# Optimization experiments

Hardware: AMD Instinct MI355X
Metric: run time of the kernel (lower is better)

Reference implementation:

```python
import jax, jax.numpy as jnp
import numpy as np


def _pairwise_sq_dist(a, b):
    # a: (B,N,D), b: (B,M,D) -> (B,N,M) squared euclidean distances
    # matmul trick matching torch.cdist (clamped at 0 before implicit sqrt)
    a2 = jnp.sum(a * a, axis=-1)  # (B,N)
    b2 = jnp.sum(b * b, axis=-1)  # (B,M)
    ab = jnp.einsum('bnd,bmd->bnm', a, b)  # (B,N,M)
    d2 = a2[:, :, None] + b2[:, None, :] - 2.0 * ab
    return jnp.maximum(d2, 0.0)


def setup_inputs() -> dict:
    key = jax.random.key(0)
    k1, k2 = jax.random.split(key)
    B, N, M, D = 8, 8192, 8192, 3
    gts = jax.random.normal(k1, (B, N, D), dtype=jnp.float32)
    preds = jax.random.normal(k2, (B, M, D), dtype=jnp.float32)
    return {"gts": gts, "preds": preds}


def reference(gts, preds):
    d2 = _pairwise_sq_dist(gts, preds)           # (B,N,M)
    min_g2p = jnp.min(d2, axis=2)                # (B,N) nearest pred for each gt
    min_p2g = jnp.min(d2, axis=1)                # (B,M) nearest gt for each pred
    return jnp.mean(min_g2p) + jnp.mean(min_p2g)
```

## Files before the change

kernel.cpp:

```cpp
#include <hip/hip_runtime.h>
#include <math.h>


#define BB 8
#define NPTS 8192
#define ROWS 512
#define CH 1024
#define NPAIR (CH / 64)

typedef __attribute__((ext_vector_type(8)))  short short8;
typedef __attribute__((ext_vector_type(16))) float float16;

#define ONE_BF16 ((short)0x3F80)

__device__ inline unsigned short bf16rn(float f) {
    unsigned int u = __float_as_uint(f);
    u += 0x7FFFu + ((u >> 16) & 1u);
    return (unsigned short)(u >> 16);
}
__device__ inline float bf2f(unsigned short h) {
    return __uint_as_float(((unsigned int)h) << 16);
}
__device__ inline float min3f(float a, float b, float c) {
    return fminf(fminf(a, b), c);
}
__device__ inline float min16(const float16 d) {
    float t0 = min3f(d[0],  d[1],  d[2]);
    float t1 = min3f(d[3],  d[4],  d[5]);
    float t2 = min3f(d[6],  d[7],  d[8]);
    float t3 = min3f(d[9],  d[10], d[11]);
    float t4 = min3f(d[12], d[13], d[14]);
    return fminf(min3f(t0, t1, t2), min3f(t3, t4, d[15]));
}

#define DPP_FMIN(v, CTRL) do {                                                \
    int _s = __builtin_amdgcn_update_dpp(__float_as_int(v), __float_as_int(v),\
                                         (CTRL), 0xf, 0xf, false);            \
    (v) = fminf((v), __int_as_float(_s)); } while (0)

__device__ inline void packB(float x, float y, float z, short8& lo, short8& hi) {
    float w = x * x + y * y + z * z;
    unsigned short xh = bf16rn(x), yh = bf16rn(y), zh = bf16rn(z);
    unsigned short xl = bf16rn(x - bf2f(xh));
    unsigned short yl = bf16rn(y - bf2f(yh));
    unsigned short zl = bf16rn(z - bf2f(zh));
    unsigned short wh = bf16rn(w), wl = bf16rn(w - bf2f(wh));
    lo[0]=(short)xh; lo[1]=(short)yh; lo[2]=(short)zh; lo[3]=(short)xl;
    lo[4]=(short)yl; lo[5]=(short)zl; lo[6]=(short)xh; lo[7]=(short)yh;
    hi[0]=(short)zh; hi[1]=ONE_BF16;  hi[2]=ONE_BF16;  hi[3]=(short)wh;
    hi[4]=(short)wl; hi[5]=0;         hi[6]=0;         hi[7]=0;
}
__device__ inline void packA(float x, float y, float z, short8& lo, short8& hi) {
    float w = x * x + y * y + z * z;
    float mx = -2.0f * x, my = -2.0f * y, mz = -2.0f * z;
    unsigned short xh = bf16rn(mx), yh = bf16rn(my), zh = bf16rn(mz);
    unsigned short xl = bf16rn(mx - bf2f(xh));
    unsigned short yl = bf16rn(my - bf2f(yh));
    unsigned short zl = bf16rn(mz - bf2f(zh));
    unsigned short wh = bf16rn(w), wl = bf16rn(w - bf2f(wh));
    lo[0]=(short)xh; lo[1]=(short)yh; lo[2]=(short)zh; lo[3]=(short)xh;
    lo[4]=(short)yh; lo[5]=(short)zh; lo[6]=(short)xl; lo[7]=(short)yl;
    hi[0]=(short)zl; hi[1]=(short)wh; hi[2]=(short)wl; hi[3]=ONE_BF16;
    hi[4]=ONE_BF16;  hi[5]=0;         hi[6]=0;         hi[7]=0;
}

__global__ __launch_bounds__(512, 4) void chamfer_main(
    const float* __restrict__ gts, const float* __restrict__ preds,
    unsigned int* __restrict__ minn, unsigned int* __restrict__ minp)
{
    __shared__ short8 sB[2][CH];

    const int b       = blockIdx.z;
    const int rowBase = blockIdx.x * ROWS;
    const int colBase = blockIdx.y * CH;
    const int tid  = threadIdx.x;
    const int lane = tid & 63;
    const int wave = tid >> 6;
    const int h    = lane >> 5;
    const int c    = lane & 31;

    for (int i = tid; i < CH; i += 512) {
        const float* p = preds + ((size_t)b * NPTS + colBase + i) * 3;
        short8 lo, hi;
        packB(p[0], p[1], p[2], lo, hi);
        sB[0][i] = lo; sB[1][i] = hi;
    }

    short8 a[2];
    {
        const float* g = gts + ((size_t)b * NPTS + rowBase + wave * 64 + c) * 3;
#pragma unroll
        for (int r = 0; r < 2; ++r) {
            short8 lo, hi;
            packA(g[r*96], g[r*96+1], g[r*96+2], lo, hi);
            a[r] = h ? hi : lo;
        }
    }

    float16 zacc;
#pragma unroll
    for (int q = 0; q < 16; ++q) zacc[q] = 0.0f;

    const float kInf = __builtin_inff();
    float rm[2][16];
#pragma unroll
    for (int r = 0; r < 2; ++r)
#pragma unroll
        for (int q = 0; q < 16; ++q) rm[r][q] = kInf;

    __syncthreads();

    unsigned int* minp_b = minp + (size_t)b * NPTS + colBase;
    const short8* myB = &sB[h][c];

#pragma unroll 2
    for (int tp = 0; tp < NPAIR; ++tp) {
        short8 b0 = myB[tp * 64];
        short8 b1 = myB[tp * 64 + 32];
        float16 d0 = __builtin_amdgcn_mfma_f32_32x32x16_bf16(a[0], b0, zacc, 0, 0, 0);
        float16 d1 = __builtin_amdgcn_mfma_f32_32x32x16_bf16(a[0], b1, zacc, 0, 0, 0);
#pragma unroll
        for (int q = 0; q < 16; ++q) rm[0][q] = min3f(rm[0][q], d0[q], d1[q]);
        float c0 = min16(d0);
        float c1 = min16(d1);
        d0 = __builtin_amdgcn_mfma_f32_32x32x16_bf16(a[1], b0, zacc, 0, 0, 0);
        d1 = __builtin_amdgcn_mfma_f32_32x32x16_bf16(a[1], b1, zacc, 0, 0, 0);
#pragma unroll
        for (int q = 0; q < 16; ++q) rm[1][q] = min3f(rm[1][q], d0[q], d1[q]);
        c0 = fminf(c0, min16(d0));
        c1 = fminf(c1, min16(d1));
        c0 = fminf(c0, __shfl_xor(c0, 32));
        c1 = fminf(c1, __shfl_xor(c1, 32));
        float cv = h ? c1 : c0;
        atomicMin(&minp_b[tp * 64 + lane], __float_as_uint(fmaxf(cv, 0.0f)));
    }

#pragma unroll
    for (int r = 0; r < 2; ++r)
#pragma unroll
        for (int q = 0; q < 16; ++q) {
            float v = rm[r][q];
            DPP_FMIN(v, 0x111);
            DPP_FMIN(v, 0x112);
            DPP_FMIN(v, 0x114);
            DPP_FMIN(v, 0x118);
            DPP_FMIN(v, 0x142);
            rm[r][q] = v;
        }
    if ((lane & 31) == 31) {
        unsigned int* mb = minn + (size_t)b * NPTS + rowBase + wave * 64;
#pragma unroll
        for (int r = 0; r < 2; ++r)
#pragma unroll
            for (int q = 0; q < 16; ++q) {
                int row = r * 32 + (q & 3) + 8 * (q >> 2) + 4 * h;
                atomicMin(&mb[row], __float_as_uint(fmaxf(rm[r][q], 0.0f)));
            }
    }
}

__global__ void chamfer_reduce(const unsigned int* __restrict__ minn,
                               const unsigned int* __restrict__ minp,
                               float* __restrict__ accum,
                               unsigned int* __restrict__ ticket,
                               float* __restrict__ out)
{
    const int idx = blockIdx.x * blockDim.x + threadIdx.x;
    const int stride = gridDim.x * blockDim.x;

    float s0 = 0.0f, s1 = 0.0f;
    for (int i = idx; i < BB * NPTS; i += stride) s0 += __uint_as_float(minn[i]);
    for (int i = idx; i < BB * NPTS; i += stride) s1 += __uint_as_float(minp[i]);

#pragma unroll
    for (int m = 1; m < 64; m <<= 1) {
        s0 += __shfl_xor(s0, m, 64);
        s1 += __shfl_xor(s1, m, 64);
    }
    __shared__ float w0[4], w1[4];
    if ((threadIdx.x & 63) == 0) {
        w0[threadIdx.x >> 6] = s0;
        w1[threadIdx.x >> 6] = s1;
    }
    __syncthreads();
    if (threadIdx.x == 0) {
        atomicAdd(&accum[0], w0[0] + w0[1] + w0[2] + w0[3]);
        atomicAdd(&accum[1], w1[0] + w1[1] + w1[2] + w1[3]);
        __threadfence();
        unsigned int old = atomicAdd(ticket, 1u);
        unsigned int G = gridDim.x;
        if (old == 0xAAAAAAAAu + G - 1u || old == G - 1u) {
            float a0 = atomicAdd(&accum[0], 0.0f);
            float a1 = atomicAdd(&accum[1], 0.0f);
            out[0] = a0 / (float)(BB * NPTS) + a1 / (float)(BB * NPTS);
        }
    }
}

extern "C" void kernel_launch(void* const* d_in, const int* in_sizes, int n_in,
                              void* d_out, int out_size, void* d_ws, size_t ws_size,
                              hipStream_t stream) {
    const float* gts   = (const float*)d_in[0];
    const float* preds = (const float*)d_in[1];
    float* out = (float*)d_out;

    unsigned int* minn   = (unsigned int*)d_ws;
    unsigned int* minp   = minn + (size_t)BB * NPTS;
    float*        accum  = (float*)(minp + (size_t)BB * NPTS);
    unsigned int* ticket = (unsigned int*)(accum + 2);

    dim3 grid(NPTS / ROWS, NPTS / CH, BB);
    chamfer_main<<<grid, 512, 0, stream>>>(gts, preds, minn, minp);

    chamfer_reduce<<<64, 256, 0, stream>>>(minn, minp, accum, ticket, out);
}
```

Measured before the change: 105.1 us.

## Compute each chamfer direction in separate blocks instead of column-min atomics

Doubles the grid so that one half of the blocks computes gt-to-pred row minima and the other half computes pred-to-gt row minima, with the roles of the two point sets swapped. This drops the per-iteration column reductions, cross-half shuffles and global atomicMin from the inner loop. In exchange, every distance tile is computed twice, doubling MFMA work. The loop unroll factor is also raised from 2 to 4.

```diff
diff --git a/kernel.cpp b/kernel.cpp
--- a/kernel.cpp
+++ b/kernel.cpp
@@ -23,14 +23,6 @@
 }
 __device__ inline float min3f(float a, float b, float c) {
     return fminf(fminf(a, b), c);
-}
-__device__ inline float min16(const float16 d) {
-    float t0 = min3f(d[0],  d[1],  d[2]);
-    float t1 = min3f(d[3],  d[4],  d[5]);
-    float t2 = min3f(d[6],  d[7],  d[8]);
-    float t3 = min3f(d[9],  d[10], d[11]);
-    float t4 = min3f(d[12], d[13], d[14]);
-    return fminf(min3f(t0, t1, t2), min3f(t3, t4, d[15]));
 }
 
 #define DPP_FMIN(v, CTRL) do {                                                \
@@ -70,7 +62,9 @@
 {
     __shared__ short8 sB[2][CH];
 
-    const int b       = blockIdx.z;
+    const int zz      = blockIdx.z;
+    const int b       = zz >> 1;
+    const int dir     = zz & 1;
     const int rowBase = blockIdx.x * ROWS;
     const int colBase = blockIdx.y * CH;
     const int tid  = threadIdx.x;
@@ -79,8 +73,12 @@
     const int h    = lane >> 5;
     const int c    = lane & 31;
 
+    const float* Arr = dir ? preds : gts;
+    const float* Brr = dir ? gts : preds;
+    unsigned int* outMin = (dir ? minp : minn) + (size_t)b * NPTS;
+
     for (int i = tid; i < CH; i += 512) {
-        const float* p = preds + ((size_t)b * NPTS + colBase + i) * 3;
+        const float* p = Brr + ((size_t)b * NPTS + colBase + i) * 3;
         short8 lo, hi;
         packB(p[0], p[1], p[2], lo, hi);
         sB[0][i] = lo; sB[1][i] = hi;
@@ -88,7 +86,7 @@
 
     short8 a[2];
     {
-        const float* g = gts + ((size_t)b * NPTS + rowBase + wave * 64 + c) * 3;
+        const float* g = Arr + ((size_t)b * NPTS + rowBase + wave * 64 + c) * 3;
 #pragma unroll
         for (int r = 0; r < 2; ++r) {
             short8 lo, hi;
@@ -110,10 +108,9 @@
 
     __syncthreads();
 
-    unsigned int* minp_b = minp + (size_t)b * NPTS + colBase;
     const short8* myB = &sB[h][c];
 
-#pragma unroll 2
+#pragma unroll 4
     for (int tp = 0; tp < NPAIR; ++tp) {
         short8 b0 = myB[tp * 64];
         short8 b1 = myB[tp * 64 + 32];
@@ -121,18 +118,10 @@
         float16 d1 = __builtin_amdgcn_mfma_f32_32x32x16_bf16(a[0], b1, zacc, 0, 0, 0);
 #pragma unroll
         for (int q = 0; q < 16; ++q) rm[0][q] = min3f(rm[0][q], d0[q], d1[q]);
-        float c0 = min16(d0);
-        float c1 = min16(d1);
-        d0 = __builtin_amdgcn_mfma_f32_32x32x16_bf16(a[1], b0, zacc, 0, 0, 0);
-        d1 = __builtin_amdgcn_mfma_f32_32x32x16_bf16(a[1], b1, zacc, 0, 0, 0);
-#pragma unroll
-        for (int q = 0; q < 16; ++q) rm[1][q] = min3f(rm[1][q], d0[q], d1[q]);
-        c0 = fminf(c0, min16(d0));
-        c1 = fminf(c1, min16(d1));
-        c0 = fminf(c0, __shfl_xor(c0, 32));
-        c1 = fminf(c1, __shfl_xor(c1, 32));
-        float cv = h ? c1 : c0;
-        atomicMin(&minp_b[tp * 64 + lane], __float_as_uint(fmaxf(cv, 0.0f)));
+        float16 d2 = __builtin_amdgcn_mfma_f32_32x32x16_bf16(a[1], b0, zacc, 0, 0, 0);
+        float16 d3 = __builtin_amdgcn_mfma_f32_32x32x16_bf16(a[1], b1, zacc, 0, 0, 0);
+#pragma unroll
+        for (int q = 0; q < 16; ++q) rm[1][q] = min3f(rm[1][q], d2[q], d3[q]);
     }
 
 #pragma unroll
@@ -148,7 +137,7 @@
             rm[r][q] = v;
         }
     if ((lane & 31) == 31) {
-        unsigned int* mb = minn + (size_t)b * NPTS + rowBase + wave * 64;
+        unsigned int* mb = outMin + rowBase + wave * 64;
 #pragma unroll
         for (int r = 0; r < 2; ++r)
 #pragma unroll
@@ -209,7 +198,7 @@
     float*        accum  = (float*)(minp + (size_t)BB * NPTS);
     unsigned int* ticket = (unsigned int*)(accum + 2);
 
-    dim3 grid(NPTS / ROWS, NPTS / CH, BB);
+    dim3 grid(NPTS / ROWS, NPTS / CH, BB * 2);
     chamfer_main<<<grid, 512, 0, stream>>>(gts, preds, minn, minp);
 
     chamfer_reduce<<<64, 256, 0, stream>>>(minn, minp, accum, ticket, out);
```

After: 112.9 us. 7.4% more time.
